# Kernel optimization log

Hardware: AMD Instinct MI355X
Metric: run time of the kernel (lower is better)

The kernel has to match this reference:

```python
import jax, jax.numpy as jnp
from jax import lax
import numpy as np

NUM_EMBEDDINGS = 512
EMBEDDING_DIM = 64
COMMITMENT_COST = 0.25
SPARSITY_LEVEL = 8


def batch_omp(data, dictionary, max_nonzero):
    """Batch-OMP (Rubinstein et al.).
    data: [D, N], dictionary: [D, K] (columns unit-norm). Returns gamma [K, N].
    Runs a fixed max_nonzero greedy steps (the torch tolerance 1e-7 never
    triggers early exit on random data).
    """
    D, N = data.shape
    K = dictionary.shape[1]
    G = dictionary.T @ dictionary                 # [K, K] Gram matrix
    h_bar = (dictionary.T @ data).T               # [N, K] initial correlations
    h = h_bar
    mask = jnp.zeros((N, K), dtype=bool)          # selected-atom indicator
    rows = jnp.arange(N)
    L = jnp.ones((N, 1, 1), dtype=data.dtype)     # incremental Cholesky of G[I,I]
    I = None                                      # [N, k] selected indices
    x = jnp.zeros((N, K), dtype=data.dtype)
    for k in range(1, max_nonzero + 1):
        # greedy atom selection (masking already-chosen atoms)
        idx = jnp.argmax(jnp.abs(h * (~mask).astype(h.dtype)), axis=1)   # [N]
        mask = mask.at[rows, idx].set(True)
        if k > 1:
            g = G[I, idx[:, None]][..., None]                            # [N, k-1, 1]
            w = lax.linalg.triangular_solve(L, g, left_side=True, lower=True)
            w = jnp.swapaxes(w, 1, 2)                                    # [N, 1, k-1]
            w_corner = jnp.sqrt(1.0 - jnp.sum(w * w, axis=2, keepdims=True))
            top = jnp.concatenate([L, jnp.zeros((N, k - 1, 1), L.dtype)], axis=2)
            bot = jnp.concatenate([w, w_corner], axis=2)
            L = jnp.concatenate([top, bot], axis=1)                      # [N, k, k]
            I = jnp.concatenate([I, idx[:, None]], axis=1)
        else:
            I = idx[:, None]
        hb = jnp.take_along_axis(h_bar, I, axis=1)[..., None]            # [N, k, 1]
        # cholesky_solve: L L^T x = hb
        y = lax.linalg.triangular_solve(L, hb, left_side=True, lower=True)
        xs = lax.linalg.triangular_solve(L, y, left_side=True, lower=True,
                                         transpose_a=True)              # [N, k, 1]
        x = jnp.zeros((N, K), data.dtype).at[rows[:, None], I].set(xs[..., 0])
        beta = x @ G                                                     # x is zero off-support
        h = h_bar - beta
    return x.T                                                           # [K, N]


def setup_inputs() -> dict:
    key = jax.random.key(0)
    k1, k2 = jax.random.split(key)
    z_e = jax.random.normal(k1, (32, EMBEDDING_DIM, 32, 32), dtype=jnp.float32)
    dictionary = jax.random.normal(k2, (EMBEDDING_DIM, NUM_EMBEDDINGS), dtype=jnp.float32)
    beta = jnp.array([1.0 - COMMITMENT_COST], dtype=jnp.float32)  # nn.Parameter(1 - commitment_cost)
    return {"z_e": z_e, "dictionary": dictionary, "beta": beta}


def reference(z_e, dictionary, beta):
    # straight-through column normalization (torch does it via .data assignment)
    Dn_val = dictionary / jnp.linalg.norm(dictionary, axis=0)
    Dn = dictionary + lax.stop_gradient(Dn_val - dictionary)
    zp = jnp.transpose(z_e, (0, 2, 3, 1))                 # [B, H, W, C]
    ze_shape = zp.shape
    zf = zp.reshape(EMBEDDING_DIM, -1)                    # view(D, -1): [D, N]
    gamma = lax.stop_gradient(batch_omp(zf, Dn, SPARSITY_LEVEL))   # [K, N]; copied via .data in torch
    recon = Dn @ gamma                                    # [D, N]
    e_latent_loss = jnp.mean((lax.stop_gradient(recon) - zf) ** 2)
    q_loss = jnp.mean((recon - lax.stop_gradient(zf)) ** 2)
    loss = e_latent_loss * COMMITMENT_COST + beta[0] * q_loss
    recon_st = zf + lax.stop_gradient(recon - zf)         # straight-through
    sm = jax.nn.softmax(gamma, axis=0)
    perplexity = jnp.exp(-jnp.mean(jnp.sum(sm * jnp.log(sm + 1e-10), axis=0)))
    recon_out = jnp.transpose(recon_st.reshape(ze_shape), (0, 3, 1, 2))
    return loss, recon_out, lax.stop_gradient(zf), perplexity, gamma
```

## Files before the change

kernel.cpp:

```cpp
#include <hip/hip_runtime.h>
#include <math.h>

#define NCOL 32768
#define KAT  512
#define DIM  64
#define CPB  16

#define O_LOSS  0
#define O_RECON 1
#define O_ZF    2097153
#define O_PERP  4194305
#define O_GAMMA 4194306

#define WS_DN   0
#define WS_DNT  32768
#define WS_G    65536
#define WS_ACC  327680

__device__ __forceinline__ float wave_max_bcast_f32(float v) {
    int x = __float_as_int(v);
    int t;
    t = __builtin_amdgcn_update_dpp(x, x, 0x111, 0xf, 0xf, false);
    x = __float_as_int(fmaxf(__int_as_float(x), __int_as_float(t)));
    t = __builtin_amdgcn_update_dpp(x, x, 0x112, 0xf, 0xf, false);
    x = __float_as_int(fmaxf(__int_as_float(x), __int_as_float(t)));
    t = __builtin_amdgcn_update_dpp(x, x, 0x114, 0xf, 0xf, false);
    x = __float_as_int(fmaxf(__int_as_float(x), __int_as_float(t)));
    t = __builtin_amdgcn_update_dpp(x, x, 0x118, 0xf, 0xf, false);
    x = __float_as_int(fmaxf(__int_as_float(x), __int_as_float(t)));
    t = __builtin_amdgcn_update_dpp(x, x, 0x142, 0xa, 0xf, false);
    x = __float_as_int(fmaxf(__int_as_float(x), __int_as_float(t)));
    t = __builtin_amdgcn_update_dpp(x, x, 0x143, 0xc, 0xf, false);
    x = __float_as_int(fmaxf(__int_as_float(x), __int_as_float(t)));
    return __int_as_float(__builtin_amdgcn_readlane(x, 63));
}

__device__ __forceinline__ unsigned wave_min_bcast_u32(unsigned v) {
    int x = (int)v;
    int t;
    t = __builtin_amdgcn_update_dpp(x, x, 0x111, 0xf, 0xf, false);
    x = (int)min((unsigned)x, (unsigned)t);
    t = __builtin_amdgcn_update_dpp(x, x, 0x112, 0xf, 0xf, false);
    x = (int)min((unsigned)x, (unsigned)t);
    t = __builtin_amdgcn_update_dpp(x, x, 0x114, 0xf, 0xf, false);
    x = (int)min((unsigned)x, (unsigned)t);
    t = __builtin_amdgcn_update_dpp(x, x, 0x118, 0xf, 0xf, false);
    x = (int)min((unsigned)x, (unsigned)t);
    t = __builtin_amdgcn_update_dpp(x, x, 0x142, 0xa, 0xf, false);
    x = (int)min((unsigned)x, (unsigned)t);
    t = __builtin_amdgcn_update_dpp(x, x, 0x143, 0xc, 0xf, false);
    x = (int)min((unsigned)x, (unsigned)t);
    return (unsigned)__builtin_amdgcn_readlane(x, 63);
}

__device__ __forceinline__ float wave_sum_bcast_f32(float v) {
    int x = __float_as_int(v);
    int t;
    t = __builtin_amdgcn_update_dpp(x, x, 0x0B1, 0xf, 0xf, false);
    x = __float_as_int(__int_as_float(x) + __int_as_float(t));
    t = __builtin_amdgcn_update_dpp(x, x, 0x04E, 0xf, 0xf, false);
    x = __float_as_int(__int_as_float(x) + __int_as_float(t));
    t = __builtin_amdgcn_update_dpp(x, x, 0x141, 0xf, 0xf, false);
    x = __float_as_int(__int_as_float(x) + __int_as_float(t));
    t = __builtin_amdgcn_update_dpp(x, x, 0x140, 0xf, 0xf, false);
    x = __float_as_int(__int_as_float(x) + __int_as_float(t));
    t = __builtin_amdgcn_update_dpp(x, x, 0x142, 0xa, 0xf, false);
    x = __float_as_int(__int_as_float(x) + __int_as_float(t));
    t = __builtin_amdgcn_update_dpp(x, x, 0x143, 0xc, 0xf, false);
    x = __float_as_int(__int_as_float(x) + __int_as_float(t));
    return __int_as_float(__builtin_amdgcn_readlane(x, 63));
}

__device__ __forceinline__ float sum8_all_f32(float v) {
    int x = __float_as_int(v);
    int t;
    t = __builtin_amdgcn_update_dpp(x, x, 0x0B1, 0xf, 0xf, false);
    x = __float_as_int(__int_as_float(x) + __int_as_float(t));
    t = __builtin_amdgcn_update_dpp(x, x, 0x04E, 0xf, 0xf, false);
    x = __float_as_int(__int_as_float(x) + __int_as_float(t));
    t = __builtin_amdgcn_update_dpp(x, x, 0x141, 0xf, 0xf, false);
    x = __float_as_int(__int_as_float(x) + __int_as_float(t));
    return __int_as_float(x);
}

__global__ void prep_kernel(const float* __restrict__ dict, float* __restrict__ ws) {
    float* Dn  = ws + WS_DN;
    float* DnT = ws + WS_DNT;
    float* acc = ws + WS_ACC;
    int a = blockIdx.x * 64 + threadIdx.x;
    if (blockIdx.x == 0 && threadIdx.x < 2) acc[threadIdx.x] = 0.f;
    float s = 0.f;
    #pragma unroll
    for (int d = 0; d < DIM; ++d) { float v = dict[d*KAT + a]; s += v * v; }
    float nrm = sqrtf(s);
    #pragma unroll
    for (int d = 0; d < DIM; ++d) {
        float v = dict[d*KAT + a] / nrm;
        Dn[d*KAT + a]  = v;
        DnT[a*DIM + d] = v;
    }
}

__global__ void gram_kernel(const float* __restrict__ ws_in, float* __restrict__ ws) {
    const float* Dn = ws_in + WS_DN;
    float* G = ws + WS_G;
    int i = blockIdx.x, j = threadIdx.x;
    float s = 0.f;
    #pragma unroll
    for (int d = 0; d < DIM; ++d)
        s = fmaf(Dn[d*KAT + i], Dn[d*KAT + j], s);
    G[i*KAT + j] = s;
}

__global__ __launch_bounds__(256) void zg_kernel(const float* __restrict__ z_e,
                                                 float* __restrict__ out) {
    __shared__ float tile[64 * 33];
    int t = threadIdx.x;
    if (blockIdx.x < 1024) {
        int s = blockIdx.x;
        int b = s >> 5, h = s & 31;
        int srcbase = b * 65536 + h * 32;
        #pragma unroll
        for (int i = 0; i < 8; ++i) {
            int e = t + i * 256;
            int c = e >> 5, w = e & 31;
            tile[c * 33 + w] = z_e[srcbase + c * 1024 + w];
        }
        __syncthreads();
        int obase = O_ZF + s * 2048;
        #pragma unroll
        for (int i = 0; i < 8; ++i) {
            int e = t + i * 256;
            out[obase + e] = tile[(e & 63) * 33 + (e >> 6)];
        }
    } else {
        float2* g2 = (float2*)(out + O_GAMMA);
        int id = (blockIdx.x - 1024) * 256 + t;
        #pragma unroll
        for (int i = 0; i < 4; ++i)
            g2[id + i * 2097152] = make_float2(0.f, 0.f);
    }
}

__global__ __launch_bounds__(256, 4) void omp_kernel(const float* __restrict__ z_e,
                                                     const float* __restrict__ ws,
                                                     float* __restrict__ out,
                                                     float* __restrict__ wsw) {
    const float* Dn  = ws + WS_DN;
    const float* DnT = ws + WS_DNT;
    const float* G   = ws + WS_G;
    float* acc = wsw + WS_ACC;

    __shared__ __align__(16) float xcols[DIM * CPB];
    __shared__ float hbar[CPB * KAT];

    const int t = threadIdx.x;
    const int n_base = blockIdx.x * CPB;

    #pragma unroll
    for (int i = 0; i < 4; ++i) {
        int e = t + i * 256;
        int d = e >> 4, c = e & 15;
        int L = d * NCOL + n_base + c;
        int src = (L >> 16) * 65536 + (L & 63) * 1024 + (((L >> 11) & 31) << 5) + ((L >> 6) & 31);
        xcols[e] = z_e[src];
    }
    __syncthreads();

    {
        float a0[16], a1[16];
        #pragma unroll
        for (int i = 0; i < 16; ++i) { a0[i] = 0.f; a1[i] = 0.f; }
        const float4* xc4 = (const float4*)xcols;
        for (int d = 0; d < DIM; ++d) {
            float v0 = Dn[d * KAT + t];
            float v1 = Dn[d * KAT + 256 + t];
            #pragma unroll
            for (int q = 0; q < 4; ++q) {
                float4 xv = xc4[d * 4 + q];
                a0[q*4+0] = fmaf(v0, xv.x, a0[q*4+0]);
                a0[q*4+1] = fmaf(v0, xv.y, a0[q*4+1]);
                a0[q*4+2] = fmaf(v0, xv.z, a0[q*4+2]);
                a0[q*4+3] = fmaf(v0, xv.w, a0[q*4+3]);
                a1[q*4+0] = fmaf(v1, xv.x, a1[q*4+0]);
                a1[q*4+1] = fmaf(v1, xv.y, a1[q*4+1]);
                a1[q*4+2] = fmaf(v1, xv.z, a1[q*4+2]);
                a1[q*4+3] = fmaf(v1, xv.w, a1[q*4+3]);
            }
        }
        #pragma unroll
        for (int c = 0; c < 16; ++c) {
            hbar[c * KAT + t]       = a0[c];
            hbar[c * KAT + 256 + t] = a1[c];
        }
    }
    __syncthreads();

    const int wv = t >> 6, lane = t & 63;
    float wv_sq = 0.f, wv_S = 0.f;

    #pragma unroll 1
    for (int cc = 0; cc < 4; ++cc) {
        const int col = wv * 4 + cc;
        const int n = n_base + col;
        const float* hbcol = hbar + col * KAT;

        float h[8];
        #pragma unroll
        for (int r = 0; r < 8; ++r) h[r] = hbcol[(r << 6) + lane];

        unsigned msk = 0;
        float uv[56];
        float Lr[28];
        float invd[8], yv[8], xr[8];
        int Iv[8];

        #pragma unroll
        for (int k = 0; k < 8; ++k) {
            float bv = -1.f; int bi = 0; float hb = 0.f;
            #pragma unroll
            for (int r = 0; r < 8; ++r) {
                float av = ((msk >> r) & 1) ? -1.f : fabsf(h[r]);
                bool gt = av > bv;
                bv = gt ? av : bv;
                bi = gt ? ((r << 6) | lane) : bi;
                hb = gt ? h[r] : hb;
            }
            float maxv = wave_max_bcast_f32(bv);
            unsigned long long tie = __ballot(bv == maxv);
            int idx; float hwin;
            if (__popcll(tie) == 1) {
                int sl = __ffsll((unsigned long long)tie) - 1;
                idx  = __builtin_amdgcn_readlane(bi, sl);
                hwin = __int_as_float(__builtin_amdgcn_readlane(__float_as_int(hb), sl));
            } else {
                unsigned cand = (bv == maxv) ? (unsigned)bi : 0xffffffffu;
                idx = (int)wave_min_bcast_u32(cand);
                unsigned long long sm = __ballot((bv == maxv) && (bi == idx) && (hb < 0.f));
                hwin = (sm != 0ull) ? -maxv : maxv;
            }

            if ((idx & 63) == lane) msk |= 1u << (idx >> 6);
            Iv[k] = idx;

            const float* grow = G + idx * KAT;
            float gk[8];
            if (k < 7) {
                #pragma unroll
                for (int r = 0; r < 8; ++r) gk[r] = grow[(r << 6) + lane];
            }

            float Lk[7];
            if (k == 0) {
                invd[0] = 1.f;
            } else {
                float s2 = 0.f;
                #pragma unroll
                for (int i = 0; i < 7; ++i) if (i < k) {
                    float a = grow[Iv[i]];
                    #pragma unroll
                    for (int j = 0; j < 7; ++j) if (j < i) a = fmaf(-Lr[i*(i-1)/2 + j], Lk[j], a);
                    Lk[i] = a * invd[i];
                    s2 = fmaf(Lk[i], Lk[i], s2);
                }
                #pragma unroll
                for (int j = 0; j < 7; ++j) if (j < k) Lr[k*(k-1)/2 + j] = Lk[j];
                invd[k] = 1.f / sqrtf(1.f - s2);
            }
            yv[k] = hwin * invd[k];

            if (k < 7) {
                #pragma unroll
                for (int r = 0; r < 8; ++r) {
                    float a = gk[r];
                    #pragma unroll
                    for (int j = 0; j < 7; ++j) if (j < k) a = fmaf(-Lk[j], uv[j*8 + r], a);
                    a *= invd[k];
                    uv[k*8 + r] = a;
                    h[r] = fmaf(-yv[k], a, h[r]);
                }
            }
        }

        #pragma unroll
        for (int i = 7; i >= 0; --i) {
            float a = yv[i];
            #pragma unroll
            for (int j = 0; j < 8; ++j) if (j > i) a = fmaf(-Lr[j*(j-1)/2 + i], xr[j], a);
            xr[i] = a * invd[i];
        }

        #pragma unroll
        for (int j = 0; j < 8; ++j)
            if (lane == j) out[O_GAMMA + Iv[j] * NCOL + n] = xr[j];

        float rec = 0.f;
        #pragma unroll
        for (int j = 0; j < 8; ++j)
            rec = fmaf(xr[j], DnT[Iv[j] * DIM + lane], rec);
        int L = lane * NCOL + n;
        int perm = (L >> 16) * 65536 + (L & 63) * 1024 + (((L >> 11) & 31) << 5) + ((L >> 6) & 31);
        out[O_RECON + perm] = rec;

        float xd = xcols[lane * CPB + col];
        float diff = rec - xd;
        wv_sq += wave_sum_bcast_f32(diff * diff);

        {
            float m = 0.f;
            #pragma unroll
            for (int j = 0; j < 8; ++j) m = fmaxf(m, xr[j]);
            float xsel = 0.f;
            #pragma unroll
            for (int j = 0; j < 8; ++j) xsel = (lane == j) ? xr[j] : xsel;
            float e = (lane < 8) ? expf(xsel - m) : 0.f;
            float se = sum8_all_f32(e);
            float e0 = expf(-m);
            float Z = fmaf(504.f, e0, se);
            float invZ = 1.f / Z;
            float p = e * invZ;
            float tq = (lane < 8) ? p * logf(p + 1e-10f) : 0.f;
            tq = sum8_all_f32(tq);
            if (lane == 0) {
                float p0 = e0 * invZ;
                wv_S += tq + 504.f * p0 * logf(p0 + 1e-10f);
            }
        }
    }

    if (lane == 0) {
        atomicAdd(&acc[0], wv_sq);
        atomicAdd(&acc[1], wv_S);
    }
}

__global__ void fin_kernel(const float* __restrict__ ws, const float* __restrict__ beta,
                           float* __restrict__ out) {
    const float* acc = ws + WS_ACC;
    float mse = acc[0] / 2097152.f;
    out[O_LOSS] = mse * 0.25f + beta[0] * mse;
    out[O_PERP] = expf(-acc[1] / 32768.f);
}

extern "C" void kernel_launch(void* const* d_in, const int* in_sizes, int n_in,
                              void* d_out, int out_size, void* d_ws, size_t ws_size,
                              hipStream_t stream) {
    const float* z_e  = (const float*)d_in[0];
    const float* dict = (const float*)d_in[1];
    const float* beta = (const float*)d_in[2];
    float* out = (float*)d_out;
    float* ws  = (float*)d_ws;

    prep_kernel<<<8, 64, 0, stream>>>(dict, ws);
    gram_kernel<<<512, 512, 0, stream>>>(ws, ws);
    zg_kernel<<<9216, 256, 0, stream>>>(z_e, out);
    omp_kernel<<<2048, 256, 0, stream>>>(z_e, ws, out, ws);
    fin_kernel<<<1, 1, 0, stream>>>(ws, beta, out);
}
```

Baseline: 357.7 us.

## Reuse projected Gram rows for Cholesky, tree argmax, fuse prep into transpose kernel

The Cholesky row entries are now taken from the already-computed orthogonalized Gram rows (uv) through a lane readlane, instead of a fresh global G lookup followed by a forward substitution. The per-lane argmax over 8 registers becomes a tree reduction, which shortens the dependency chain. The dictionary normalization is merged into the z_e transpose/gamma-zeroing kernel, removing one launch. The h_bar load and store are vectorized to float2, which changes the atom mapping per thread to interleaved pairs.

```diff
diff --git a/kernel.cpp b/kernel.cpp
--- a/kernel.cpp
+++ b/kernel.cpp
@@ -83,21 +83,51 @@
     return __int_as_float(x);
 }
 
-__global__ void prep_kernel(const float* __restrict__ dict, float* __restrict__ ws) {
-    float* Dn  = ws + WS_DN;
-    float* DnT = ws + WS_DNT;
-    float* acc = ws + WS_ACC;
-    int a = blockIdx.x * 64 + threadIdx.x;
-    if (blockIdx.x == 0 && threadIdx.x < 2) acc[threadIdx.x] = 0.f;
-    float s = 0.f;
-    #pragma unroll
-    for (int d = 0; d < DIM; ++d) { float v = dict[d*KAT + a]; s += v * v; }
-    float nrm = sqrtf(s);
-    #pragma unroll
-    for (int d = 0; d < DIM; ++d) {
-        float v = dict[d*KAT + a] / nrm;
-        Dn[d*KAT + a]  = v;
-        DnT[a*DIM + d] = v;
+__global__ __launch_bounds__(256) void zgp_kernel(const float* __restrict__ z_e,
+                                                  const float* __restrict__ dict,
+                                                  float* __restrict__ out,
+                                                  float* __restrict__ ws) {
+    __shared__ float tile[64 * 33];
+    int t = threadIdx.x;
+    if (blockIdx.x < 1024) {
+        int s = blockIdx.x;
+        int b = s >> 5, h = s & 31;
+        int srcbase = b * 65536 + h * 32;
+        #pragma unroll
+        for (int i = 0; i < 8; ++i) {
+            int e = t + i * 256;
+            int c = e >> 5, w = e & 31;
+            tile[c * 33 + w] = z_e[srcbase + c * 1024 + w];
+        }
+        __syncthreads();
+        int obase = O_ZF + s * 2048;
+        #pragma unroll
+        for (int i = 0; i < 8; ++i) {
+            int e = t + i * 256;
+            out[obase + e] = tile[(e & 63) * 33 + (e >> 6)];
+        }
+    } else if (blockIdx.x < 9216) {
+        float2* g2 = (float2*)(out + O_GAMMA);
+        int id = (blockIdx.x - 1024) * 256 + t;
+        #pragma unroll
+        for (int i = 0; i < 4; ++i)
+            g2[id + i * 2097152] = make_float2(0.f, 0.f);
+    } else {
+        float* Dn  = ws + WS_DN;
+        float* DnT = ws + WS_DNT;
+        float* acc = ws + WS_ACC;
+        int a = (blockIdx.x - 9216) * 256 + t;
+        if (blockIdx.x == 9216 && t < 2) acc[t] = 0.f;
+        float s = 0.f;
+        #pragma unroll
+        for (int d = 0; d < DIM; ++d) { float v = dict[d*KAT + a]; s += v * v; }
+        float nrm = sqrtf(s);
+        #pragma unroll
+        for (int d = 0; d < DIM; ++d) {
+            float v = dict[d*KAT + a] / nrm;
+            Dn[d*KAT + a]  = v;
+            DnT[a*DIM + d] = v;
+        }
     }
 }
 
@@ -112,36 +142,6 @@
     G[i*KAT + j] = s;
 }
 
-__global__ __launch_bounds__(256) void zg_kernel(const float* __restrict__ z_e,
-                                                 float* __restrict__ out) {
-    __shared__ float tile[64 * 33];
-    int t = threadIdx.x;
-    if (blockIdx.x < 1024) {
-        int s = blockIdx.x;
-        int b = s >> 5, h = s & 31;
-        int srcbase = b * 65536 + h * 32;
-        #pragma unroll
-        for (int i = 0; i < 8; ++i) {
-            int e = t + i * 256;
-            int c = e >> 5, w = e & 31;
-            tile[c * 33 + w] = z_e[srcbase + c * 1024 + w];
-        }
-        __syncthreads();
-        int obase = O_ZF + s * 2048;
-        #pragma unroll
-        for (int i = 0; i < 8; ++i) {
-            int e = t + i * 256;
-            out[obase + e] = tile[(e & 63) * 33 + (e >> 6)];
-        }
-    } else {
-        float2* g2 = (float2*)(out + O_GAMMA);
-        int id = (blockIdx.x - 1024) * 256 + t;
-        #pragma unroll
-        for (int i = 0; i < 4; ++i)
-            g2[id + i * 2097152] = make_float2(0.f, 0.f);
-    }
-}
-
 __global__ __launch_bounds__(256, 4) void omp_kernel(const float* __restrict__ z_e,
                                                      const float* __restrict__ ws,
                                                      float* __restrict__ out,
@@ -171,28 +171,27 @@
         float a0[16], a1[16];
         #pragma unroll
         for (int i = 0; i < 16; ++i) { a0[i] = 0.f; a1[i] = 0.f; }
+        const float2* Dn2 = (const float2*)Dn;
         const float4* xc4 = (const float4*)xcols;
         for (int d = 0; d < DIM; ++d) {
-            float v0 = Dn[d * KAT + t];
-            float v1 = Dn[d * KAT + 256 + t];
+            float2 v = Dn2[d * 256 + t];
             #pragma unroll
             for (int q = 0; q < 4; ++q) {
                 float4 xv = xc4[d * 4 + q];
-                a0[q*4+0] = fmaf(v0, xv.x, a0[q*4+0]);
-                a0[q*4+1] = fmaf(v0, xv.y, a0[q*4+1]);
-                a0[q*4+2] = fmaf(v0, xv.z, a0[q*4+2]);
-                a0[q*4+3] = fmaf(v0, xv.w, a0[q*4+3]);
-                a1[q*4+0] = fmaf(v1, xv.x, a1[q*4+0]);
-                a1[q*4+1] = fmaf(v1, xv.y, a1[q*4+1]);
-                a1[q*4+2] = fmaf(v1, xv.z, a1[q*4+2]);
-                a1[q*4+3] = fmaf(v1, xv.w, a1[q*4+3]);
-            }
-        }
-        #pragma unroll
-        for (int c = 0; c < 16; ++c) {
-            hbar[c * KAT + t]       = a0[c];
-            hbar[c * KAT + 256 + t] = a1[c];
-        }
+                a0[q*4+0] = fmaf(v.x, xv.x, a0[q*4+0]);
+                a0[q*4+1] = fmaf(v.x, xv.y, a0[q*4+1]);
+                a0[q*4+2] = fmaf(v.x, xv.z, a0[q*4+2]);
+                a0[q*4+3] = fmaf(v.x, xv.w, a0[q*4+3]);
+                a1[q*4+0] = fmaf(v.y, xv.x, a1[q*4+0]);
+                a1[q*4+1] = fmaf(v.y, xv.y, a1[q*4+1]);
+                a1[q*4+2] = fmaf(v.y, xv.z, a1[q*4+2]);
+                a1[q*4+3] = fmaf(v.y, xv.w, a1[q*4+3]);
+            }
+        }
+        float2* hb2 = (float2*)hbar;
+        #pragma unroll
+        for (int c = 0; c < 16; ++c)
+            hb2[c * 256 + t] = make_float2(a0[c], a1[c]);
     }
     __syncthreads();
 
@@ -217,15 +216,27 @@
 
         #pragma unroll
         for (int k = 0; k < 8; ++k) {
-            float bv = -1.f; int bi = 0; float hb = 0.f;
+            float tv[8]; int ti[8]; float th[8];
             #pragma unroll
             for (int r = 0; r < 8; ++r) {
-                float av = ((msk >> r) & 1) ? -1.f : fabsf(h[r]);
-                bool gt = av > bv;
-                bv = gt ? av : bv;
-                bi = gt ? ((r << 6) | lane) : bi;
-                hb = gt ? h[r] : hb;
-            }
+                tv[r] = ((msk >> r) & 1) ? -1.f : fabsf(h[r]);
+                ti[r] = r;
+                th[r] = h[r];
+            }
+            #pragma unroll
+            for (int s = 1; s < 8; s <<= 1) {
+                #pragma unroll
+                for (int r = 0; r < 8; r += 2 * s) {
+                    bool c = tv[r + s] > tv[r];
+                    tv[r] = c ? tv[r + s] : tv[r];
+                    ti[r] = c ? ti[r + s] : ti[r];
+                    th[r] = c ? th[r + s] : th[r];
+                }
+            }
+            float bv = tv[0];
+            int   bi = (ti[0] << 6) | lane;
+            float hb = th[0];
+
             float maxv = wave_max_bcast_f32(bv);
             unsigned long long tie = __ballot(bv == maxv);
             int idx; float hwin;
@@ -242,6 +253,7 @@
 
             if ((idx & 63) == lane) msk |= 1u << (idx >> 6);
             Iv[k] = idx;
+            const int rsel = idx >> 6, lsel = idx & 63;
 
             const float* grow = G + idx * KAT;
             float gk[8];
@@ -257,11 +269,14 @@
                 float s2 = 0.f;
                 #pragma unroll
                 for (int i = 0; i < 7; ++i) if (i < k) {
-                    float a = grow[Iv[i]];
+                    float wsel = uv[i*8 + 0];
                     #pragma unroll
-                    for (int j = 0; j < 7; ++j) if (j < i) a = fmaf(-Lr[i*(i-1)/2 + j], Lk[j], a);
-                    Lk[i] = a * invd[i];
-                    s2 = fmaf(Lk[i], Lk[i], s2);
+                    for (int r = 1; r < 8; ++r)
+                        wsel = (rsel == r) ? uv[i*8 + r] : wsel;
+                    float w = __int_as_float(
+                        __builtin_amdgcn_readlane(__float_as_int(wsel), lsel));
+                    Lk[i] = w;
+                    s2 = fmaf(w, w, s2);
                 }
                 #pragma unroll
                 for (int j = 0; j < 7; ++j) if (j < k) Lr[k*(k-1)/2 + j] = Lk[j];
@@ -351,9 +366,8 @@
     float* out = (float*)d_out;
     float* ws  = (float*)d_ws;
 
-    prep_kernel<<<8, 64, 0, stream>>>(dict, ws);
+    zgp_kernel<<<9218, 256, 0, stream>>>(z_e, dict, out, ws);
     gram_kernel<<<512, 512, 0, stream>>>(ws, ws);
-    zg_kernel<<<9216, 256, 0, stream>>>(z_e, out);
     omp_kernel<<<2048, 256, 0, stream>>>(z_e, ws, out, ws);
     fin_kernel<<<1, 1, 0, stream>>>(ws, beta, out);
 }
```

New measurement: 402.0 us. 12.4% more time.
